# Performance work log

Hardware: AMD Instinct MI355X
Metric: run time of the kernel (lower is better)

## Reference

```python
import jax, jax.numpy as jnp
import numpy as np

N = 50000   # nodes
E = 800000  # edges
F = 256     # in_channels
H = 256     # hidden (GCN output)


def setup_inputs() -> dict:
    key = jax.random.key(0)
    ks = jax.random.split(key, 6)
    x = jax.random.normal(ks[0], (N, F), jnp.float32)
    edge_index = jax.random.randint(ks[1], (2, E), 0, N)
    perm = jax.random.permutation(ks[2], N)
    W = jax.random.normal(ks[3], (F, H), jnp.float32) / np.sqrt(F)
    b = jnp.zeros((H,), jnp.float32)
    a = jnp.full((1,), 0.25, jnp.float32)  # PReLU slope
    disc_W = jax.random.normal(ks[4], (H, H), jnp.float32) / np.sqrt(H)
    return {"x": x, "W": W, "b": b, "a": a, "disc_W": disc_W,
            "edge_index": edge_index, "perm": perm}


def _gcn(x, W, b, src, dst, n):
    # GCNConv: linear -> symmetric-normalized aggregation (with self-loops) -> bias
    xw = x @ W  # [N, H]
    loop = jnp.arange(n)
    s = jnp.concatenate([src, loop])
    d = jnp.concatenate([dst, loop])
    ew = jnp.ones(s.shape[0], xw.dtype)
    deg = jax.ops.segment_sum(ew, d, num_segments=n)          # [N]
    dinv = jnp.where(deg > 0, jax.lax.rsqrt(deg), 0.0)
    norm = dinv[s] * dinv[d]                                   # [E+N]
    out = jax.ops.segment_sum(xw[s] * norm[:, None], d, num_segments=n)
    return out + b


def reference(x, W, b, a, disc_W, edge_index, perm):
    src, dst = edge_index[0], edge_index[1]
    n = x.shape[0]

    def encode(feat):
        h = _gcn(feat, W, b, src, dst, n)
        return jnp.where(h >= 0, h, a * h)  # PReLU

    z1 = encode(x)          # clean
    z2 = encode(x[perm])    # corrupted (row permutation)
    summary = jax.nn.sigmoid(z1.mean(axis=0))  # [H]
    wsum = disc_W @ summary                     # [H]
    pos = z1 @ wsum  # [N]
    neg = z2 @ wsum  # [N]
    return pos, neg
```

## Files before the change

kernel.cpp:

```cpp
#include <hip/hip_runtime.h>

#define N_NODES 50000
#define N_EDGES 800000
#define DIM 256
#define NB 196
#define UNROLL 8
#define MAXE (N_EDGES + N_NODES * UNROLL)
#define CSB 512

typedef __attribute__((ext_vector_type(8))) short bf16x8;
typedef __attribute__((ext_vector_type(4))) float f32x4;

__device__ __forceinline__ unsigned int f2bf(float f) {
  unsigned int u = __float_as_uint(f);
  return (u + 0x7FFFu + ((u >> 16) & 1u)) >> 16;
}
__device__ __forceinline__ float bf_lo(unsigned int u) {
  return __uint_as_float(u << 16);
}
__device__ __forceinline__ float bf_hi(unsigned int u) {
  return __uint_as_float(u & 0xFFFF0000u);
}


__global__ void k_deg(const int* __restrict__ dst, int* __restrict__ deg) {
  int e = blockIdx.x * blockDim.x + threadIdx.x;
  if (e < N_EDGES) atomicAdd(&deg[dst[e]], 1);
}

__global__ __launch_bounds__(256) void k_bsum(const int* __restrict__ deg,
                                              float* __restrict__ dinv,
                                              int* __restrict__ bsum) {
  __shared__ int red[4];
  const int t = threadIdx.x;
  const int i = blockIdx.x * 256 + t;
  int pd = 0;
  if (i < N_NODES) {
    int d = deg[i];
    dinv[i] = rsqrtf((float)(d + 1));
    pd = (d + UNROLL - 1) & ~(UNROLL - 1);
  }
  int s = pd;
#pragma unroll
  for (int off = 32; off > 0; off >>= 1) s += __shfl_down(s, off);
  if ((t & 63) == 0) red[t >> 6] = s;
  __syncthreads();
  if (t == 0) bsum[blockIdx.x] = red[0] + red[1] + red[2] + red[3];
}

__global__ __launch_bounds__(256) void k_bscan(const int* __restrict__ bsum,
                                               int* __restrict__ boff,
                                               int* __restrict__ row_start) {
  __shared__ int s[256];
  const int t = threadIdx.x;
  int v = (t < NB) ? bsum[t] : 0;
  s[t] = v;
  __syncthreads();
  for (int off = 1; off < 256; off <<= 1) {
    int u = (t >= off) ? s[t - off] : 0;
    __syncthreads();
    s[t] += u;
    __syncthreads();
  }
  if (t < NB) boff[t] = s[t] - v;
  if (t == NB - 1) row_start[N_NODES] = s[NB - 1];
}

__global__ __launch_bounds__(256) void k_rowstart(const int* __restrict__ deg,
                                                  const int* __restrict__ boff,
                                                  int* __restrict__ row_start,
                                                  int* __restrict__ cursor) {
  __shared__ int s[256];
  const int t = threadIdx.x;
  const int i = blockIdx.x * 256 + t;
  int pd = (i < N_NODES) ? ((deg[i] + UNROLL - 1) & ~(UNROLL - 1)) : 0;
  s[t] = pd;
  __syncthreads();
  for (int off = 1; off < 256; off <<= 1) {
    int u = (t >= off) ? s[t - off] : 0;
    __syncthreads();
    s[t] += u;
    __syncthreads();
  }
  if (i < N_NODES) {
    int r = boff[blockIdx.x] + s[t] - pd;
    row_start[i] = r;
    cursor[i] = r;
  }
}

__global__ void k_scatter(const int* __restrict__ src, const int* __restrict__ dst,
                          const int* __restrict__ perm, const float* __restrict__ dinv,
                          int* __restrict__ cursor, uint2* __restrict__ meta1,
                          uint2* __restrict__ meta2) {
  int e = blockIdx.x * blockDim.x + threadIdx.x;
  if (e < N_EDGES) {
    int s = src[e], d = dst[e];
    int p = atomicAdd(&cursor[d], 1);
    unsigned int nrm = __float_as_uint(dinv[s] * dinv[d]);
    meta1[p] = make_uint2((unsigned)s, nrm);
    meta2[p] = make_uint2((unsigned)perm[s], nrm);
  }
}


__global__ void k_prep(const float* __restrict__ W, ushort* __restrict__ Wt) {
  int n = blockIdx.x, k = threadIdx.x;
  Wt[n * DIM + k] = (ushort)f2bf(W[k * DIM + n]);
}


__global__ __launch_bounds__(512) void k_gemm(const float* __restrict__ X,
                                              const ushort* __restrict__ Wt,
                                              ushort* __restrict__ XW) {
  __shared__ ushort Xs[128 * 40];
  __shared__ ushort Ws[256 * 40];
  const int tid = threadIdx.x;
  const int lane = tid & 63;
  const int w = tid >> 6;
  const int wm = w >> 2, wn = w & 3;
  const int m0 = blockIdx.x * 128;
  const int l16 = lane & 15, kh = lane >> 4;

  f32x4 acc[4][4];
#pragma unroll
  for (int mf = 0; mf < 4; ++mf)
#pragma unroll
    for (int nf = 0; nf < 4; ++nf) acc[mf][nf] = (f32x4){0.f, 0.f, 0.f, 0.f};

  for (int k0 = 0; k0 < DIM; k0 += 32) {
#pragma unroll
    for (int it = 0; it < 2; ++it) {
      int idx = tid + it * 512;
      int row = idx >> 3, q = idx & 7;
      int grow = m0 + row;
      float4 v = make_float4(0.f, 0.f, 0.f, 0.f);
      if (grow < N_NODES)
        v = *reinterpret_cast<const float4*>(&X[(size_t)grow * DIM + k0 + q * 4]);
      uint2 p;
      p.x = f2bf(v.x) | (f2bf(v.y) << 16);
      p.y = f2bf(v.z) | (f2bf(v.w) << 16);
      *reinterpret_cast<uint2*>(&Xs[row * 40 + q * 4]) = p;
    }
#pragma unroll
    for (int it = 0; it < 2; ++it) {
      int idx = tid + it * 512;
      int n = idx >> 2, c = idx & 3;
      uint4 wv = *reinterpret_cast<const uint4*>(&Wt[n * DIM + k0 + c * 8]);
      *reinterpret_cast<uint4*>(&Ws[n * 40 + c * 8]) = wv;
    }
    __syncthreads();
    bf16x8 a[4], b[4];
#pragma unroll
    for (int f = 0; f < 4; ++f) {
      a[f] = *reinterpret_cast<const bf16x8*>(&Ws[(wn * 64 + f * 16 + l16) * 40 + kh * 8]);
      b[f] = *reinterpret_cast<const bf16x8*>(&Xs[(wm * 64 + f * 16 + l16) * 40 + kh * 8]);
    }
#pragma unroll
    for (int mf = 0; mf < 4; ++mf)
#pragma unroll
      for (int nf = 0; nf < 4; ++nf)
        acc[mf][nf] = __builtin_amdgcn_mfma_f32_16x16x32_bf16(a[nf], b[mf],
                                                              acc[mf][nf], 0, 0, 0);
    __syncthreads();
  }
#pragma unroll
  for (int mf = 0; mf < 4; ++mf) {
    int m = m0 + wm * 64 + mf * 16 + l16;
    if (m >= N_NODES) continue;
#pragma unroll
    for (int nf = 0; nf < 4; ++nf) {
      int nb = wn * 64 + nf * 16 + kh * 4;
      uint2 p;
      p.x = f2bf(acc[mf][nf][0]) | (f2bf(acc[mf][nf][1]) << 16);
      p.y = f2bf(acc[mf][nf][2]) | (f2bf(acc[mf][nf][3]) << 16);
      *reinterpret_cast<uint2*>(&XW[(size_t)m * DIM + nb]) = p;
    }
  }
}


struct Acc8 { float a[8]; };

__device__ __forceinline__ void fma8(Acc8& A, uint4 v, float n) {
  A.a[0] = fmaf(bf_lo(v.x), n, A.a[0]);
  A.a[1] = fmaf(bf_hi(v.x), n, A.a[1]);
  A.a[2] = fmaf(bf_lo(v.y), n, A.a[2]);
  A.a[3] = fmaf(bf_hi(v.y), n, A.a[3]);
  A.a[4] = fmaf(bf_lo(v.z), n, A.a[4]);
  A.a[5] = fmaf(bf_hi(v.z), n, A.a[5]);
  A.a[6] = fmaf(bf_lo(v.w), n, A.a[6]);
  A.a[7] = fmaf(bf_hi(v.w), n, A.a[7]);
}

__device__ __forceinline__ void agg_ell(const ushort* __restrict__ xw,
                                        const uint2* __restrict__ meta,
                                        int e0, int e1, int c, Acc8& A) {
  for (int e = e0; e < e1; e += UNROLL) {
    uint2 m[UNROLL];
#pragma unroll
    for (int j = 0; j < UNROLL; ++j) m[j] = meta[e + j];
    uint4 v[UNROLL];
#pragma unroll
    for (int j = 0; j < UNROLL; ++j)
      v[j] = *reinterpret_cast<const uint4*>(xw + (size_t)m[j].x * DIM + c * 8);
#pragma unroll
    for (int j = 0; j < UNROLL; ++j) fma8(A, v[j], __uint_as_float(m[j].y));
  }
}

__device__ __forceinline__ void epilogue8(Acc8& A, const float* __restrict__ bias,
                                          float a0, int c) {
  float4 b0 = *reinterpret_cast<const float4*>(&bias[c * 8]);
  float4 b1 = *reinterpret_cast<const float4*>(&bias[c * 8 + 4]);
  A.a[0] += b0.x; A.a[1] += b0.y; A.a[2] += b0.z; A.a[3] += b0.w;
  A.a[4] += b1.x; A.a[5] += b1.y; A.a[6] += b1.z; A.a[7] += b1.w;
#pragma unroll
  for (int j = 0; j < 8; ++j) A.a[j] = A.a[j] >= 0.f ? A.a[j] : a0 * A.a[j];
}

__global__ __launch_bounds__(256) void k_agg1(
    const ushort* __restrict__ xw, const int* __restrict__ row_start,
    const uint2* __restrict__ meta1, const float* __restrict__ dinv,
    const float* __restrict__ bias, const float* __restrict__ slope,
    ushort* __restrict__ z1) {
  const int tid = threadIdx.x;
  const int lane = tid & 63;
  const int h = lane >> 5, c = lane & 31;
  const int r = ((blockIdx.x * 256 + tid) >> 6) * 2 + h;
  const float di = dinv[r];
  Acc8 A;
#pragma unroll
  for (int j = 0; j < 8; ++j) A.a[j] = 0.f;
  uint4 sv = *reinterpret_cast<const uint4*>(xw + (size_t)r * DIM + c * 8);
  fma8(A, sv, di * di);
  agg_ell(xw, meta1, row_start[r], row_start[r + 1], c, A);
  epilogue8(A, bias, slope[0], c);
  uint4 p;
  p.x = f2bf(A.a[0]) | (f2bf(A.a[1]) << 16);
  p.y = f2bf(A.a[2]) | (f2bf(A.a[3]) << 16);
  p.z = f2bf(A.a[4]) | (f2bf(A.a[5]) << 16);
  p.w = f2bf(A.a[6]) | (f2bf(A.a[7]) << 16);
  *reinterpret_cast<uint4*>(z1 + (size_t)r * DIM + c * 8) = p;
}

__global__ __launch_bounds__(256) void k_agg2_negpos(
    const ushort* __restrict__ xw, const ushort* __restrict__ z1,
    const int* __restrict__ row_start, const uint2* __restrict__ meta2,
    const int* __restrict__ perm, const float* __restrict__ dinv,
    const float* __restrict__ bias, const float* __restrict__ slope,
    const float* __restrict__ wsum, float* __restrict__ pos,
    float* __restrict__ neg) {
  const int tid = threadIdx.x;
  const int lane = tid & 63;
  const int h = lane >> 5, c = lane & 31;
  const int r = ((blockIdx.x * 256 + tid) >> 6) * 2 + h;
  const float di = dinv[r];
  Acc8 A;
#pragma unroll
  for (int j = 0; j < 8; ++j) A.a[j] = 0.f;
  uint4 sv = *reinterpret_cast<const uint4*>(xw + (size_t)perm[r] * DIM + c * 8);
  fma8(A, sv, di * di);
  agg_ell(xw, meta2, row_start[r], row_start[r + 1], c, A);
  epilogue8(A, bias, slope[0], c);
  float4 w0 = *reinterpret_cast<const float4*>(&wsum[c * 8]);
  float4 w1 = *reinterpret_cast<const float4*>(&wsum[c * 8 + 4]);
  float dn = A.a[0] * w0.x + A.a[1] * w0.y + A.a[2] * w0.z + A.a[3] * w0.w +
             A.a[4] * w1.x + A.a[5] * w1.y + A.a[6] * w1.z + A.a[7] * w1.w;
  uint4 zv = *reinterpret_cast<const uint4*>(z1 + (size_t)r * DIM + c * 8);
  float dp = bf_lo(zv.x) * w0.x + bf_hi(zv.x) * w0.y +
             bf_lo(zv.y) * w0.z + bf_hi(zv.y) * w0.w +
             bf_lo(zv.z) * w1.x + bf_hi(zv.z) * w1.y +
             bf_lo(zv.w) * w1.z + bf_hi(zv.w) * w1.w;
#pragma unroll
  for (int off = 16; off > 0; off >>= 1) {
    dn += __shfl_down(dn, off, 32);
    dp += __shfl_down(dp, off, 32);
  }
  if (c == 0) { neg[r] = dn; pos[r] = dp; }
}


__global__ __launch_bounds__(256) void k_colsum(const ushort* __restrict__ z1,
                                                float* __restrict__ partial) {
  __shared__ float red[8 * 256];
  const int t = threadIdx.x;
  const int c8 = t & 31;
  const int g = t >> 5;
  float s[8] = {0.f, 0.f, 0.f, 0.f, 0.f, 0.f, 0.f, 0.f};
  for (int r = blockIdx.x * 8 + g; r < N_NODES; r += 8 * CSB) {
    uint4 v = *reinterpret_cast<const uint4*>(z1 + (size_t)r * DIM + c8 * 8);
    s[0] += bf_lo(v.x); s[1] += bf_hi(v.x);
    s[2] += bf_lo(v.y); s[3] += bf_hi(v.y);
    s[4] += bf_lo(v.z); s[5] += bf_hi(v.z);
    s[6] += bf_lo(v.w); s[7] += bf_hi(v.w);
  }
#pragma unroll
  for (int j = 0; j < 8; ++j) red[g * 256 + c8 * 8 + j] = s[j];
  __syncthreads();
  float tot = 0.f;
#pragma unroll
  for (int g2 = 0; g2 < 8; ++g2) tot += red[g2 * 256 + t];
  partial[blockIdx.x * 256 + t] = tot;
}

__global__ __launch_bounds__(256) void k_wsum(const float* __restrict__ partial,
                                              const float* __restrict__ disc_W,
                                              float* __restrict__ wsum) {
  __shared__ float s[DIM];
  const int t = threadIdx.x;
  float a0 = 0.f, a1 = 0.f, a2 = 0.f, a3 = 0.f;
  for (int b = 0; b < CSB; b += 4) {
    a0 += partial[(b + 0) * 256 + t];
    a1 += partial[(b + 1) * 256 + t];
    a2 += partial[(b + 2) * 256 + t];
    a3 += partial[(b + 3) * 256 + t];
  }
  float m = (a0 + a1 + a2 + a3) * (1.0f / (float)N_NODES);
  s[t] = 1.0f / (1.0f + expf(-m));
  __syncthreads();
  float acc = 0.f;
  for (int j = 0; j < DIM; j += 4) {
    float4 w4 = *reinterpret_cast<const float4*>(&disc_W[t * DIM + j]);
    acc += w4.x * s[j] + w4.y * s[j + 1] + w4.z * s[j + 2] + w4.w * s[j + 3];
  }
  wsum[t] = acc;
}


extern "C" void kernel_launch(void* const* d_in, const int* in_sizes, int n_in,
                              void* d_out, int out_size, void* d_ws, size_t ws_size,
                              hipStream_t stream) {
  const float* x      = (const float*)d_in[0];
  const float* W      = (const float*)d_in[1];
  const float* b      = (const float*)d_in[2];
  const float* a      = (const float*)d_in[3];
  const float* disc_W = (const float*)d_in[4];
  const int*   eidx   = (const int*)d_in[5];
  const int*   perm   = (const int*)d_in[6];
  const int* src = eidx;
  const int* dst = eidx + N_EDGES;

  constexpr size_t SZ_BFM  = (size_t)N_NODES * DIM * 2;
  constexpr size_t SZ_META = (size_t)MAXE * 8;
  constexpr size_t OFF_XW  = 0;
  constexpr size_t OFF_Z1  = OFF_XW + SZ_BFM;
  constexpr size_t OFF_WT  = OFF_Z1 + SZ_BFM;
  constexpr size_t OFF_DEG = OFF_WT + 131072;
  constexpr size_t OFF_DNV = OFF_DEG + 200192;
  constexpr size_t OFF_RS  = OFF_DNV + 200192;
  constexpr size_t OFF_CUR = OFF_RS + 200448;
  constexpr size_t OFF_M1  = OFF_CUR + 200192;
  constexpr size_t OFF_M2  = OFF_M1 + SZ_META;
  constexpr size_t OFF_WSM = OFF_M2 + SZ_META;
  constexpr size_t OFF_BS  = OFF_WSM + 1024;
  constexpr size_t OFF_BO  = OFF_BS + 1024;
  constexpr size_t OFF_PT  = OFF_BO + 1024;
  constexpr size_t NEED    = OFF_PT + (size_t)CSB * 256 * 4;
  if (ws_size < NEED) return;

  char* ws = (char*)d_ws;
  ushort* xw     = (ushort*)(ws + OFF_XW);
  ushort* z1     = (ushort*)(ws + OFF_Z1);
  ushort* Wt     = (ushort*)(ws + OFF_WT);
  int*    deg    = (int*)(ws + OFF_DEG);
  float*  dinv   = (float*)(ws + OFF_DNV);
  int*    rowst  = (int*)(ws + OFF_RS);
  int*    cursor = (int*)(ws + OFF_CUR);
  uint2*  meta1  = (uint2*)(ws + OFF_M1);
  uint2*  meta2  = (uint2*)(ws + OFF_M2);
  float*  wsum   = (float*)(ws + OFF_WSM);
  int*    bsum   = (int*)(ws + OFF_BS);
  int*    boff   = (int*)(ws + OFF_BO);
  float*  partial= (float*)(ws + OFF_PT);

  float* pos = (float*)d_out;
  float* neg = pos + N_NODES;

  hipMemsetAsync(deg, 0, N_NODES * sizeof(int), stream);
  hipMemsetAsync(meta1, 0, SZ_META, stream);
  hipMemsetAsync(meta2, 0, SZ_META, stream);

  k_deg<<<(N_EDGES + 255) / 256, 256, 0, stream>>>(dst, deg);
  k_bsum<<<NB, 256, 0, stream>>>(deg, dinv, bsum);
  k_bscan<<<1, 256, 0, stream>>>(bsum, boff, rowst);
  k_rowstart<<<NB, 256, 0, stream>>>(deg, boff, rowst, cursor);
  k_scatter<<<(N_EDGES + 255) / 256, 256, 0, stream>>>(src, dst, perm, dinv,
                                                       cursor, meta1, meta2);

  k_prep<<<DIM, DIM, 0, stream>>>(W, Wt);
  k_gemm<<<(N_NODES + 127) / 128, 512, 0, stream>>>(x, Wt, xw);

  k_agg1<<<N_NODES / 8, 256, 0, stream>>>(xw, rowst, meta1, dinv, b, a, z1);
  k_colsum<<<CSB, 256, 0, stream>>>(z1, partial);
  k_wsum<<<1, 256, 0, stream>>>(partial, disc_W, wsum);
  k_agg2_negpos<<<N_NODES / 8, 256, 0, stream>>>(xw, z1, rowst, meta2, perm,
                                                 dinv, b, a, wsum, pos, neg);
}
```

Baseline: 269.7 us.

## Column-chunk XW layout and fuse clean and corrupted aggregation into one pass

The GEMM output is stored in eight column chunks of 32 columns, so each aggregation block gathers from a 3.2 MB slice that can stay in cache. One combined kernel aggregates both the clean and the permuted encoder using a single metadata array that packs the source and perm[source] indices as 16-bit halves. The pos/neg dot products move to a separate lightweight kernel that reads z1 and z2. In exchange, a full z2 buffer is written and read back, each edge's metadata is fetched once per chunk (eight times overall), and the 16-bit packing of perm[s] relies on node ids staying below 65536.

```diff
diff --git a/kernel.cpp b/kernel.cpp
--- a/kernel.cpp
+++ b/kernel.cpp
@@ -7,6 +7,11 @@
 #define UNROLL 8
 #define MAXE (N_EDGES + N_NODES * UNROLL)
 #define CSB 512
+#define NCH 8
+#define CCOLS 32
+#define CHSZ (N_NODES * CCOLS)
+#define RPB 16
+#define CHB (N_NODES / RPB)
 
 typedef __attribute__((ext_vector_type(8))) short bf16x8;
 typedef __attribute__((ext_vector_type(4))) float f32x4;
@@ -91,15 +96,13 @@
 
 __global__ void k_scatter(const int* __restrict__ src, const int* __restrict__ dst,
                           const int* __restrict__ perm, const float* __restrict__ dinv,
-                          int* __restrict__ cursor, uint2* __restrict__ meta1,
-                          uint2* __restrict__ meta2) {
+                          int* __restrict__ cursor, uint2* __restrict__ meta) {
   int e = blockIdx.x * blockDim.x + threadIdx.x;
   if (e < N_EDGES) {
     int s = src[e], d = dst[e];
     int p = atomicAdd(&cursor[d], 1);
-    unsigned int nrm = __float_as_uint(dinv[s] * dinv[d]);
-    meta1[p] = make_uint2((unsigned)s, nrm);
-    meta2[p] = make_uint2((unsigned)perm[s], nrm);
+    meta[p] = make_uint2((unsigned)s | ((unsigned)perm[s] << 16),
+                         __float_as_uint(dinv[s] * dinv[d]));
   }
 }
 
@@ -112,7 +115,7 @@
 
 __global__ __launch_bounds__(512) void k_gemm(const float* __restrict__ X,
                                               const ushort* __restrict__ Wt,
-                                              ushort* __restrict__ XW) {
+                                              ushort* __restrict__ XWC) {
   __shared__ ushort Xs[128 * 40];
   __shared__ ushort Ws[256 * 40];
   const int tid = threadIdx.x;
@@ -174,110 +177,90 @@
       uint2 p;
       p.x = f2bf(acc[mf][nf][0]) | (f2bf(acc[mf][nf][1]) << 16);
       p.y = f2bf(acc[mf][nf][2]) | (f2bf(acc[mf][nf][3]) << 16);
-      *reinterpret_cast<uint2*>(&XW[(size_t)m * DIM + nb]) = p;
+      *reinterpret_cast<uint2*>(&XWC[(size_t)(nb >> 5) * CHSZ + (size_t)m * CCOLS + (nb & 31)]) = p;
     }
   }
 }
 
 
-struct Acc8 { float a[8]; };
-
-__device__ __forceinline__ void fma8(Acc8& A, uint4 v, float n) {
-  A.a[0] = fmaf(bf_lo(v.x), n, A.a[0]);
-  A.a[1] = fmaf(bf_hi(v.x), n, A.a[1]);
-  A.a[2] = fmaf(bf_lo(v.y), n, A.a[2]);
-  A.a[3] = fmaf(bf_hi(v.y), n, A.a[3]);
-  A.a[4] = fmaf(bf_lo(v.z), n, A.a[4]);
-  A.a[5] = fmaf(bf_hi(v.z), n, A.a[5]);
-  A.a[6] = fmaf(bf_lo(v.w), n, A.a[6]);
-  A.a[7] = fmaf(bf_hi(v.w), n, A.a[7]);
-}
-
-__device__ __forceinline__ void agg_ell(const ushort* __restrict__ xw,
-                                        const uint2* __restrict__ meta,
-                                        int e0, int e1, int c, Acc8& A) {
-  for (int e = e0; e < e1; e += UNROLL) {
-    uint2 m[UNROLL];
-#pragma unroll
-    for (int j = 0; j < UNROLL; ++j) m[j] = meta[e + j];
-    uint4 v[UNROLL];
-#pragma unroll
-    for (int j = 0; j < UNROLL; ++j)
-      v[j] = *reinterpret_cast<const uint4*>(xw + (size_t)m[j].x * DIM + c * 8);
-#pragma unroll
-    for (int j = 0; j < UNROLL; ++j) fma8(A, v[j], __uint_as_float(m[j].y));
-  }
-}
-
-__device__ __forceinline__ void epilogue8(Acc8& A, const float* __restrict__ bias,
-                                          float a0, int c) {
-  float4 b0 = *reinterpret_cast<const float4*>(&bias[c * 8]);
-  float4 b1 = *reinterpret_cast<const float4*>(&bias[c * 8 + 4]);
-  A.a[0] += b0.x; A.a[1] += b0.y; A.a[2] += b0.z; A.a[3] += b0.w;
-  A.a[4] += b1.x; A.a[5] += b1.y; A.a[6] += b1.z; A.a[7] += b1.w;
-#pragma unroll
-  for (int j = 0; j < 8; ++j) A.a[j] = A.a[j] >= 0.f ? A.a[j] : a0 * A.a[j];
-}
-
-__global__ __launch_bounds__(256) void k_agg1(
-    const ushort* __restrict__ xw, const int* __restrict__ row_start,
-    const uint2* __restrict__ meta1, const float* __restrict__ dinv,
-    const float* __restrict__ bias, const float* __restrict__ slope,
-    ushort* __restrict__ z1) {
+__device__ __forceinline__ void fma8(float* A, uint4 v, float n) {
+  A[0] = fmaf(bf_lo(v.x), n, A[0]);
+  A[1] = fmaf(bf_hi(v.x), n, A[1]);
+  A[2] = fmaf(bf_lo(v.y), n, A[2]);
+  A[3] = fmaf(bf_hi(v.y), n, A[3]);
+  A[4] = fmaf(bf_lo(v.z), n, A[4]);
+  A[5] = fmaf(bf_hi(v.z), n, A[5]);
+  A[6] = fmaf(bf_lo(v.w), n, A[6]);
+  A[7] = fmaf(bf_hi(v.w), n, A[7]);
+}
+
+__global__ __launch_bounds__(256) void k_aggc(
+    const ushort* __restrict__ xwc, const int* __restrict__ row_start,
+    const uint2* __restrict__ meta, const int* __restrict__ perm,
+    const float* __restrict__ dinv, const float* __restrict__ bias,
+    const float* __restrict__ slope, ushort* __restrict__ z1,
+    ushort* __restrict__ z2) {
+  const int blk = blockIdx.x;
+  const int ch = blk / CHB;
+  const int rb = blk % CHB;
   const int tid = threadIdx.x;
-  const int lane = tid & 63;
-  const int h = lane >> 5, c = lane & 31;
-  const int r = ((blockIdx.x * 256 + tid) >> 6) * 2 + h;
-  const float di = dinv[r];
-  Acc8 A;
-#pragma unroll
-  for (int j = 0; j < 8; ++j) A.a[j] = 0.f;
-  uint4 sv = *reinterpret_cast<const uint4*>(xw + (size_t)r * DIM + c * 8);
-  fma8(A, sv, di * di);
-  agg_ell(xw, meta1, row_start[r], row_start[r + 1], c, A);
-  epilogue8(A, bias, slope[0], c);
-  uint4 p;
-  p.x = f2bf(A.a[0]) | (f2bf(A.a[1]) << 16);
-  p.y = f2bf(A.a[2]) | (f2bf(A.a[3]) << 16);
-  p.z = f2bf(A.a[4]) | (f2bf(A.a[5]) << 16);
-  p.w = f2bf(A.a[6]) | (f2bf(A.a[7]) << 16);
-  *reinterpret_cast<uint4*>(z1 + (size_t)r * DIM + c * 8) = p;
-}
-
-__global__ __launch_bounds__(256) void k_agg2_negpos(
-    const ushort* __restrict__ xw, const ushort* __restrict__ z1,
-    const int* __restrict__ row_start, const uint2* __restrict__ meta2,
-    const int* __restrict__ perm, const float* __restrict__ dinv,
-    const float* __restrict__ bias, const float* __restrict__ slope,
-    const float* __restrict__ wsum, float* __restrict__ pos,
-    float* __restrict__ neg) {
-  const int tid = threadIdx.x;
-  const int lane = tid & 63;
-  const int h = lane >> 5, c = lane & 31;
-  const int r = ((blockIdx.x * 256 + tid) >> 6) * 2 + h;
-  const float di = dinv[r];
-  Acc8 A;
-#pragma unroll
-  for (int j = 0; j < 8; ++j) A.a[j] = 0.f;
-  uint4 sv = *reinterpret_cast<const uint4*>(xw + (size_t)perm[r] * DIM + c * 8);
-  fma8(A, sv, di * di);
-  agg_ell(xw, meta2, row_start[r], row_start[r + 1], c, A);
-  epilogue8(A, bias, slope[0], c);
-  float4 w0 = *reinterpret_cast<const float4*>(&wsum[c * 8]);
-  float4 w1 = *reinterpret_cast<const float4*>(&wsum[c * 8 + 4]);
-  float dn = A.a[0] * w0.x + A.a[1] * w0.y + A.a[2] * w0.z + A.a[3] * w0.w +
-             A.a[4] * w1.x + A.a[5] * w1.y + A.a[6] * w1.z + A.a[7] * w1.w;
-  uint4 zv = *reinterpret_cast<const uint4*>(z1 + (size_t)r * DIM + c * 8);
-  float dp = bf_lo(zv.x) * w0.x + bf_hi(zv.x) * w0.y +
-             bf_lo(zv.y) * w0.z + bf_hi(zv.y) * w0.w +
-             bf_lo(zv.z) * w1.x + bf_hi(zv.z) * w1.y +
-             bf_lo(zv.w) * w1.z + bf_hi(zv.w) * w1.w;
-#pragma unroll
-  for (int off = 16; off > 0; off >>= 1) {
-    dn += __shfl_down(dn, off, 32);
-    dp += __shfl_down(dp, off, 32);
-  }
-  if (c == 0) { neg[r] = dn; pos[r] = dp; }
+  const int r = rb * RPB + (tid >> 4);
+  const int l = tid & 15;
+  const int eg = l >> 2;
+  const int sc = l & 3;
+  const ushort* xc = xwc + (size_t)ch * CHSZ;
+
+  float a1[8] = {0.f, 0.f, 0.f, 0.f, 0.f, 0.f, 0.f, 0.f};
+  float a2[8] = {0.f, 0.f, 0.f, 0.f, 0.f, 0.f, 0.f, 0.f};
+  const int e1 = row_start[r + 1];
+  for (int e = row_start[r]; e < e1; e += 8) {
+    uint4 mm = *reinterpret_cast<const uint4*>(meta + e + eg * 2);
+    uint4 vA1 = *reinterpret_cast<const uint4*>(xc + (size_t)(mm.x & 0xFFFFu) * CCOLS + sc * 8);
+    uint4 vA2 = *reinterpret_cast<const uint4*>(xc + (size_t)(mm.x >> 16) * CCOLS + sc * 8);
+    uint4 vB1 = *reinterpret_cast<const uint4*>(xc + (size_t)(mm.z & 0xFFFFu) * CCOLS + sc * 8);
+    uint4 vB2 = *reinterpret_cast<const uint4*>(xc + (size_t)(mm.z >> 16) * CCOLS + sc * 8);
+    const float nA = __uint_as_float(mm.y), nB = __uint_as_float(mm.w);
+    fma8(a1, vA1, nA); fma8(a2, vA2, nA);
+    fma8(a1, vB1, nB); fma8(a2, vB2, nB);
+  }
+#pragma unroll
+  for (int j = 0; j < 8; ++j) {
+    a1[j] += __shfl_xor(a1[j], 4); a2[j] += __shfl_xor(a2[j], 4);
+    a1[j] += __shfl_xor(a1[j], 8); a2[j] += __shfl_xor(a2[j], 8);
+  }
+  if (eg == 0) {
+    const float di = dinv[r];
+    const float d2 = di * di;
+    const int pr = perm[r];
+    uint4 s1 = *reinterpret_cast<const uint4*>(xc + (size_t)r * CCOLS + sc * 8);
+    uint4 s2 = *reinterpret_cast<const uint4*>(xc + (size_t)pr * CCOLS + sc * 8);
+    fma8(a1, s1, d2); fma8(a2, s2, d2);
+    const float* bp = bias + ch * CCOLS + sc * 8;
+    float4 b0 = *reinterpret_cast<const float4*>(bp);
+    float4 b1 = *reinterpret_cast<const float4*>(bp + 4);
+    a1[0] += b0.x; a1[1] += b0.y; a1[2] += b0.z; a1[3] += b0.w;
+    a1[4] += b1.x; a1[5] += b1.y; a1[6] += b1.z; a1[7] += b1.w;
+    a2[0] += b0.x; a2[1] += b0.y; a2[2] += b0.z; a2[3] += b0.w;
+    a2[4] += b1.x; a2[5] += b1.y; a2[6] += b1.z; a2[7] += b1.w;
+    const float a0 = slope[0];
+#pragma unroll
+    for (int j = 0; j < 8; ++j) {
+      a1[j] = a1[j] >= 0.f ? a1[j] : a0 * a1[j];
+      a2[j] = a2[j] >= 0.f ? a2[j] : a0 * a2[j];
+    }
+    uint4 p1, p2;
+    p1.x = f2bf(a1[0]) | (f2bf(a1[1]) << 16);
+    p1.y = f2bf(a1[2]) | (f2bf(a1[3]) << 16);
+    p1.z = f2bf(a1[4]) | (f2bf(a1[5]) << 16);
+    p1.w = f2bf(a1[6]) | (f2bf(a1[7]) << 16);
+    p2.x = f2bf(a2[0]) | (f2bf(a2[1]) << 16);
+    p2.y = f2bf(a2[2]) | (f2bf(a2[3]) << 16);
+    p2.z = f2bf(a2[4]) | (f2bf(a2[5]) << 16);
+    p2.w = f2bf(a2[6]) | (f2bf(a2[7]) << 16);
+    const size_t o = (size_t)r * DIM + ch * CCOLS + sc * 8;
+    *reinterpret_cast<uint4*>(z1 + o) = p1;
+    *reinterpret_cast<uint4*>(z2 + o) = p2;
+  }
 }
 
 
@@ -328,6 +311,28 @@
 }
 
 
+__global__ __launch_bounds__(256) void k_posneg(const ushort* __restrict__ z1,
+                                                const ushort* __restrict__ z2,
+                                                const float* __restrict__ wsum,
+                                                float* __restrict__ pos,
+                                                float* __restrict__ neg) {
+  const int wid = (blockIdx.x * blockDim.x + threadIdx.x) >> 6;
+  const int lane = threadIdx.x & 63;
+  if (wid >= N_NODES) return;
+  uint2 v1 = *reinterpret_cast<const uint2*>(z1 + (size_t)wid * DIM + lane * 4);
+  uint2 v2 = *reinterpret_cast<const uint2*>(z2 + (size_t)wid * DIM + lane * 4);
+  float4 w4 = *reinterpret_cast<const float4*>(&wsum[lane * 4]);
+  float dp = bf_lo(v1.x) * w4.x + bf_hi(v1.x) * w4.y + bf_lo(v1.y) * w4.z + bf_hi(v1.y) * w4.w;
+  float dn = bf_lo(v2.x) * w4.x + bf_hi(v2.x) * w4.y + bf_lo(v2.y) * w4.z + bf_hi(v2.y) * w4.w;
+#pragma unroll
+  for (int off = 32; off > 0; off >>= 1) {
+    dp += __shfl_down(dp, off);
+    dn += __shfl_down(dn, off);
+  }
+  if (lane == 0) { pos[wid] = dp; neg[wid] = dn; }
+}
+
+
 extern "C" void kernel_launch(void* const* d_in, const int* in_sizes, int n_in,
                               void* d_out, int out_size, void* d_ws, size_t ws_size,
                               hipStream_t stream) {
@@ -343,16 +348,16 @@
 
   constexpr size_t SZ_BFM  = (size_t)N_NODES * DIM * 2;
   constexpr size_t SZ_META = (size_t)MAXE * 8;
-  constexpr size_t OFF_XW  = 0;
-  constexpr size_t OFF_Z1  = OFF_XW + SZ_BFM;
-  constexpr size_t OFF_WT  = OFF_Z1 + SZ_BFM;
+  constexpr size_t OFF_XWC = 0;
+  constexpr size_t OFF_Z1  = OFF_XWC + SZ_BFM;
+  constexpr size_t OFF_Z2  = OFF_Z1 + SZ_BFM;
+  constexpr size_t OFF_WT  = OFF_Z2 + SZ_BFM;
   constexpr size_t OFF_DEG = OFF_WT + 131072;
   constexpr size_t OFF_DNV = OFF_DEG + 200192;
   constexpr size_t OFF_RS  = OFF_DNV + 200192;
   constexpr size_t OFF_CUR = OFF_RS + 200448;
-  constexpr size_t OFF_M1  = OFF_CUR + 200192;
-  constexpr size_t OFF_M2  = OFF_M1 + SZ_META;
-  constexpr size_t OFF_WSM = OFF_M2 + SZ_META;
+  constexpr size_t OFF_MT  = OFF_CUR + 200192;
+  constexpr size_t OFF_WSM = OFF_MT + SZ_META;
   constexpr size_t OFF_BS  = OFF_WSM + 1024;
   constexpr size_t OFF_BO  = OFF_BS + 1024;
   constexpr size_t OFF_PT  = OFF_BO + 1024;
@@ -360,15 +365,15 @@
   if (ws_size < NEED) return;
 
   char* ws = (char*)d_ws;
-  ushort* xw     = (ushort*)(ws + OFF_XW);
+  ushort* xwc    = (ushort*)(ws + OFF_XWC);
   ushort* z1     = (ushort*)(ws + OFF_Z1);
+  ushort* z2     = (ushort*)(ws + OFF_Z2);
   ushort* Wt     = (ushort*)(ws + OFF_WT);
   int*    deg    = (int*)(ws + OFF_DEG);
   float*  dinv   = (float*)(ws + OFF_DNV);
   int*    rowst  = (int*)(ws + OFF_RS);
   int*    cursor = (int*)(ws + OFF_CUR);
-  uint2*  meta1  = (uint2*)(ws + OFF_M1);
-  uint2*  meta2  = (uint2*)(ws + OFF_M2);
+  uint2*  meta   = (uint2*)(ws + OFF_MT);
   float*  wsum   = (float*)(ws + OFF_WSM);
   int*    bsum   = (int*)(ws + OFF_BS);
   int*    boff   = (int*)(ws + OFF_BO);
@@ -378,22 +383,21 @@
   float* neg = pos + N_NODES;
 
   hipMemsetAsync(deg, 0, N_NODES * sizeof(int), stream);
-  hipMemsetAsync(meta1, 0, SZ_META, stream);
-  hipMemsetAsync(meta2, 0, SZ_META, stream);
+  hipMemsetAsync(meta, 0, SZ_META, stream);
 
   k_deg<<<(N_EDGES + 255) / 256, 256, 0, stream>>>(dst, deg);
   k_bsum<<<NB, 256, 0, stream>>>(deg, dinv, bsum);
   k_bscan<<<1, 256, 0, stream>>>(bsum, boff, rowst);
   k_rowstart<<<NB, 256, 0, stream>>>(deg, boff, rowst, cursor);
   k_scatter<<<(N_EDGES + 255) / 256, 256, 0, stream>>>(src, dst, perm, dinv,
-                                                       cursor, meta1, meta2);
+                                                       cursor, meta);
 
   k_prep<<<DIM, DIM, 0, stream>>>(W, Wt);
-  k_gemm<<<(N_NODES + 127) / 128, 512, 0, stream>>>(x, Wt, xw);
-
-  k_agg1<<<N_NODES / 8, 256, 0, stream>>>(xw, rowst, meta1, dinv, b, a, z1);
+  k_gemm<<<(N_NODES + 127) / 128, 512, 0, stream>>>(x, Wt, xwc);
+
+  k_aggc<<<NCH * CHB, 256, 0, stream>>>(xwc, rowst, meta, perm, dinv, b, a, z1, z2);
+
   k_colsum<<<CSB, 256, 0, stream>>>(z1, partial);
   k_wsum<<<1, 256, 0, stream>>>(partial, disc_W, wsum);
-  k_agg2_negpos<<<N_NODES / 8, 256, 0, stream>>>(xw, z1, rowst, meta2, perm,
-                                                 dinv, b, a, wsum, pos, neg);
-}
+  k_posneg<<<(N_NODES * 64 + 255) / 256, 256, 0, stream>>>(z1, z2, wsum, pos, neg);
+}
```

Result: faster. 247.5 us (-8.2%).
